# Kernel optimization log

Measured on AMD Instinct MI355X. Metric: run time of the kernel, lower is better.

The kernel has to match this reference:

```python
import jax, jax.numpy as jnp
import numpy as np

N_NODES = 100000
N_EDGES = 1600000
NUM_GRAPHS = 2000
IN_CH, HID = 5, 64
NEG_SLOPE = 0.2


def _lin_params(key, out_d, in_d, bias=True):
    k1, k2 = jax.random.split(key)
    bound = 1.0 / np.sqrt(in_d)
    W = jax.random.uniform(k1, (out_d, in_d), jnp.float32, -bound, bound)
    if bias:
        b = jax.random.uniform(k2, (out_d,), jnp.float32, -bound, bound)
        return W, b
    return (W,)


def setup_inputs() -> dict:
    key = jax.random.key(0)
    ks = jax.random.split(key, 12)
    x = jax.random.normal(ks[0], (N_NODES, IN_CH), jnp.float32)
    edge_index = jax.random.randint(ks[1], (2, N_EDGES), 0, N_NODES, jnp.int64)
    batch = (jnp.arange(N_NODES, dtype=jnp.int64) * NUM_GRAPHS) // N_NODES  # 50 nodes/graph, sorted
    # SAGEConv params: lin_l (on aggregated neighbors, with bias), lin_r (root, no bias)
    W1l, b1 = _lin_params(ks[2], HID, IN_CH)
    (W1r,) = _lin_params(ks[3], HID, IN_CH, bias=False)
    W2l, b2 = _lin_params(ks[4], 2 * HID, HID)
    (W2r,) = _lin_params(ks[5], 2 * HID, HID, bias=False)
    W3l, b3 = _lin_params(ks[6], 4 * HID, 2 * HID)
    (W3r,) = _lin_params(ks[7], 4 * HID, 2 * HID, bias=False)
    # classifier MLP: 512 -> 128 -> 64 -> 1
    Wc1, bc1 = _lin_params(ks[8], 2 * HID, 8 * HID)
    Wc2, bc2 = _lin_params(ks[9], HID, 2 * HID)
    Wc3, bc3 = _lin_params(ks[10], 1, HID)
    return {
        "x": x, "edge_index": edge_index, "batch": batch, "num_graphs": NUM_GRAPHS,
        "W1l": W1l, "b1": b1, "W1r": W1r,
        "W2l": W2l, "b2": b2, "W2r": W2r,
        "W3l": W3l, "b3": b3, "W3r": W3r,
        "Wc1": Wc1, "bc1": bc1, "Wc2": Wc2, "bc2": bc2, "Wc3": Wc3, "bc3": bc3,
    }


def _sage_conv(x, src, dst, Wl, b, Wr):
    # mean-aggregate messages x[src] at dst, then lin_l(agg) + lin_r(x)
    n = x.shape[0]
    s = jax.ops.segment_sum(x[src], dst, num_segments=n)
    cnt = jax.ops.segment_sum(jnp.ones((src.shape[0],), x.dtype), dst, num_segments=n)
    mean = s / jnp.maximum(cnt, 1.0)[:, None]
    return mean @ Wl.T + b + x @ Wr.T


def reference(x, edge_index, batch, num_graphs,
              W1l, b1, W1r, W2l, b2, W2r, W3l, b3, W3r,
              Wc1, bc1, Wc2, bc2, Wc3, bc3):
    src, dst = edge_index[0], edge_index[1]
    lrelu = lambda h: jax.nn.leaky_relu(h, NEG_SLOPE)
    h = lrelu(_sage_conv(x, src, dst, W1l, b1, W1r))
    h = lrelu(_sage_conv(h, src, dst, W2l, b2, W2r))
    h = lrelu(_sage_conv(h, src, dst, W3l, b3, W3r))
    # global mean + max pool per graph -> [G, 512]
    s = jax.ops.segment_sum(h, batch, num_segments=num_graphs)
    cnt = jax.ops.segment_sum(jnp.ones((h.shape[0],), h.dtype), batch, num_segments=num_graphs)
    mean_p = s / jnp.maximum(cnt, 1.0)[:, None]
    max_p = jax.ops.segment_max(h, batch, num_segments=num_graphs)
    g = jnp.concatenate([mean_p, max_p], axis=1)
    # classifier (dropout = identity in eval mode)
    g = lrelu(g @ Wc1.T + bc1)
    g = lrelu(g @ Wc2.T + bc2)
    logits = g @ Wc3.T + bc3
    return logits.squeeze(-1)
```

## Files before the change

kernel.cpp:

```cpp
#include <hip/hip_runtime.h>
#include <cstdint>
#include <cstddef>

#define NEG_SLOPE 0.2f

typedef __attribute__((ext_vector_type(8))) short bh8;
typedef __attribute__((ext_vector_type(16))) float f32x16;

__device__ inline void splitf(float x, short& hi, short& lo) {
    uint32_t u = __float_as_uint(x);
    uint32_t rh = (u + 0x7FFFu + ((u >> 16) & 1u)) & 0xFFFF0000u;
    hi = (short)(rh >> 16);
    float rem = x - __uint_as_float(rh);
    uint32_t u2 = __float_as_uint(rem);
    lo = (short)((u2 + 0x7FFFu + ((u2 >> 16) & 1u)) >> 16);
}

__global__ void sentinel_kernel(float* __restrict__ out, int n) {
    int i = blockIdx.x * blockDim.x + threadIdx.x;
    if (i < n) out[i] = 12345.0f;
}

#define HIST_CH 8192
__global__ void bucket_count_kernel(const int* __restrict__ dst, int* __restrict__ bcnt,
                                    int ne, int nb) {
    __shared__ int hist[256];
    const int tid = threadIdx.x;
    hist[tid] = 0;
    __syncthreads();
    int e0 = blockIdx.x * HIST_CH;
    for (int i = tid; i < HIST_CH; i += 256) {
        int e = e0 + i;
        if (e < ne) atomicAdd(&hist[dst[e] >> 9], 1);
    }
    __syncthreads();
    if (tid < nb && hist[tid] > 0) atomicAdd(&bcnt[tid], hist[tid]);
}

__global__ void scan256_kernel(const int* __restrict__ bcnt, int* __restrict__ boff, int n) {
    const int tid = threadIdx.x, lane = tid & 63, wid = tid >> 6;
    __shared__ int wt[4];
    int v = (tid < n) ? bcnt[tid] : 0;
    int incl = v;
    #pragma unroll
    for (int o = 1; o < 64; o <<= 1) {
        int t = __shfl_up(incl, o);
        if (lane >= o) incl += t;
    }
    if (lane == 63) wt[wid] = incl;
    __syncthreads();
    if (tid < 4) {
        int w = wt[tid], winc = w;
        #pragma unroll
        for (int o = 1; o < 4; o <<= 1) {
            int t = __shfl_up(winc, o);
            if (tid >= o) winc += t;
        }
        wt[tid] = winc - w;
    }
    __syncthreads();
    int excl = wt[wid] + incl - v;
    if (tid < n) boff[tid] = excl;
    if (tid == n - 1) boff[n] = excl + v;
}

#define SCAT_CH 4096
__global__ void bucket_scatter_kernel(const int* __restrict__ src, const int* __restrict__ dst,
                                      const int* __restrict__ boff, int* __restrict__ bcur,
                                      unsigned* __restrict__ pairs, int ne, int nb) {
    __shared__ int hist[256], lcur[256], gbase[256];
    const int tid = threadIdx.x;
    hist[tid] = 0; lcur[tid] = 0;
    __syncthreads();
    int e0 = blockIdx.x * SCAT_CH;
    for (int i = tid; i < SCAT_CH; i += 256) {
        int e = e0 + i;
        if (e < ne) atomicAdd(&hist[dst[e] >> 9], 1);
    }
    __syncthreads();
    if (tid < nb) {
        int h = hist[tid];
        gbase[tid] = (h > 0) ? (boff[tid] + atomicAdd(&bcur[tid], h)) : 0;
    }
    __syncthreads();
    for (int i = tid; i < SCAT_CH; i += 256) {
        int e = e0 + i;
        if (e < ne) {
            int d = dst[e];
            int b = d >> 9;
            int r = atomicAdd(&lcur[b], 1);
            pairs[gbase[b] + r] = ((unsigned)(d & 511) << 17) | (unsigned)src[e];
        }
    }
}

__global__ __launch_bounds__(512) void bucket_sort_kernel(
        const unsigned* __restrict__ pairs, const int* __restrict__ boff,
        int* __restrict__ off, int* __restrict__ csr, int n_nodes) {
    __shared__ int cnt[512], lcur[512];
    __shared__ int wt[8];
    const int b = blockIdx.x;
    const int tid = threadIdx.x, lane = tid & 63, wid = tid >> 6;
    const int s = boff[b], t = boff[b + 1];
    cnt[tid] = 0; lcur[tid] = 0;
    __syncthreads();
    for (int i = s + tid; i < t; i += 512)
        atomicAdd(&cnt[pairs[i] >> 17], 1);
    __syncthreads();
    int v = cnt[tid];
    int incl = v;
    #pragma unroll
    for (int o = 1; o < 64; o <<= 1) {
        int tt = __shfl_up(incl, o);
        if (lane >= o) incl += tt;
    }
    if (lane == 63) wt[wid] = incl;
    __syncthreads();
    if (tid < 8) {
        int w = wt[tid], winc = w;
        #pragma unroll
        for (int o = 1; o < 8; o <<= 1) {
            int tt = __shfl_up(winc, o);
            if (tid >= o) winc += tt;
        }
        wt[tid] = winc - w;
    }
    __syncthreads();
    int excl = wt[wid] + incl - v;
    __syncthreads();
    cnt[tid] = excl;
    int node = b * 512 + tid;
    if (node < n_nodes) off[node] = s + excl;
    if (b == 0 && tid == 0) off[n_nodes] = boff[gridDim.x];
    __syncthreads();
    for (int i = s + tid; i < t; i += 512) {
        unsigned p = pairs[i];
        int bin = p >> 17;
        int r = atomicAdd(&lcur[bin], 1);
        csr[s + cnt[bin] + r] = (int)(p & 0x1FFFFu);
    }
}

__global__ void pack_wsplit_kernel(const float* __restrict__ Wl, const float* __restrict__ Wr,
                                   short* __restrict__ Whi, short* __restrict__ Wlo,
                                   int COUT, int K, int CIN) {
    int i = blockIdx.x * blockDim.x + threadIdx.x;
    if (i >= COUT * K) return;
    int n = i / K, k = i % K;
    float v = (k < CIN) ? Wl[n * CIN + k] : Wr[n * CIN + (k - CIN)];
    short h, l;
    splitf(v, h, l);
    Whi[i] = h; Wlo[i] = l;
}

__global__ __launch_bounds__(256) void sage1_kernel(
        const float* __restrict__ x, const int* __restrict__ off,
        const int* __restrict__ csr, const float* __restrict__ W1l,
        const float* __restrict__ W1r, const float* __restrict__ b1,
        unsigned short* __restrict__ h1hi, unsigned short* __restrict__ h1lo,
        int n_nodes) {
    __shared__ float sWl[320], sWr[320], sb[64];
    const int tid = threadIdx.x;
    for (int i = tid; i < 320; i += 256) { sWl[i] = W1l[i]; sWr[i] = W1r[i]; }
    if (tid < 64) sb[tid] = b1[tid];
    __syncthreads();
    int node = blockIdx.x * 4 + (tid >> 6);
    int lane = tid & 63;
    if (node >= n_nodes) return;
    int slot = lane >> 3, cg = lane & 7;
    int e0 = off[node], cnt = off[node + 1] - e0;
    float a0 = 0.f, a1 = 0.f;
    int i = slot;
    for (; i + 8 < cnt; i += 16) {
        int s0 = csr[e0 + i];
        int s1 = csr[e0 + i + 8];
        a0 += (cg < 5) ? x[(size_t)s0 * 5 + cg] : 0.f;
        a1 += (cg < 5) ? x[(size_t)s1 * 5 + cg] : 0.f;
    }
    for (; i < cnt; i += 8) {
        int s = csr[e0 + i];
        a0 += (cg < 5) ? x[(size_t)s * 5 + cg] : 0.f;
    }
    float acc = a0 + a1;
    #pragma unroll
    for (int o = 8; o < 64; o <<= 1) acc += __shfl_xor(acc, o);
    float inv = (cnt > 0) ? 1.f / (float)cnt : 0.f;
    float m = acc * inv;
    float xv = (lane < 5) ? x[(size_t)node * 5 + lane] : 0.f;
    float o = sb[lane];
    #pragma unroll
    for (int c = 0; c < 5; ++c) {
        o += sWl[lane * 5 + c] * __shfl(m, c);
        o += sWr[lane * 5 + c] * __shfl(xv, c);
    }
    o = o > 0.f ? o : o * NEG_SLOPE;
    short h, l;
    splitf(o, h, l);
    h1hi[(size_t)node * 64 + lane] = (unsigned short)h;
    h1lo[(size_t)node * 64 + lane] = (unsigned short)l;
}

template<int CIN>
__global__ void agg_bf16_kernel(const unsigned short* __restrict__ hb,
                                const int* __restrict__ off, const int* __restrict__ csr,
                                unsigned short* __restrict__ mhi,
                                unsigned short* __restrict__ mlo, int n_nodes) {
    constexpr int LPR = CIN / 8;
    constexpr int SLOTS = 64 / LPR;
    constexpr int UN = 16 / SLOTS;
    int node = blockIdx.x * (blockDim.x >> 6) + (threadIdx.x >> 6);
    int lane = threadIdx.x & 63;
    if (node >= n_nodes) return;
    int slot = lane / LPR, cg = lane % LPR;
    int e0 = off[node], cnt = off[node + 1] - e0;
    const unsigned short* base = hb + cg * 8;
    float acc[UN][8];
    #pragma unroll
    for (int u = 0; u < UN; ++u)
        #pragma unroll
        for (int k = 0; k < 8; ++k) acc[u][k] = 0.f;
    int i = slot;
    for (; i + (UN - 1) * SLOTS < cnt; i += UN * SLOTS) {
        int s[UN];
        #pragma unroll
        for (int u = 0; u < UN; ++u) s[u] = csr[e0 + i + u * SLOTS];
        uint4 v[UN];
        #pragma unroll
        for (int u = 0; u < UN; ++u)
            v[u] = *(const uint4*)(base + (size_t)s[u] * CIN);
        #pragma unroll
        for (int u = 0; u < UN; ++u) {
            unsigned w0 = v[u].x, w1 = v[u].y, w2 = v[u].z, w3 = v[u].w;
            acc[u][0] += __uint_as_float(w0 << 16);
            acc[u][1] += __uint_as_float(w0 & 0xFFFF0000u);
            acc[u][2] += __uint_as_float(w1 << 16);
            acc[u][3] += __uint_as_float(w1 & 0xFFFF0000u);
            acc[u][4] += __uint_as_float(w2 << 16);
            acc[u][5] += __uint_as_float(w2 & 0xFFFF0000u);
            acc[u][6] += __uint_as_float(w3 << 16);
            acc[u][7] += __uint_as_float(w3 & 0xFFFF0000u);
        }
    }
    for (; i < cnt; i += SLOTS) {
        uint4 v = *(const uint4*)(base + (size_t)csr[e0 + i] * CIN);
        unsigned w0 = v.x, w1 = v.y, w2 = v.z, w3 = v.w;
        acc[0][0] += __uint_as_float(w0 << 16);
        acc[0][1] += __uint_as_float(w0 & 0xFFFF0000u);
        acc[0][2] += __uint_as_float(w1 << 16);
        acc[0][3] += __uint_as_float(w1 & 0xFFFF0000u);
        acc[0][4] += __uint_as_float(w2 << 16);
        acc[0][5] += __uint_as_float(w2 & 0xFFFF0000u);
        acc[0][6] += __uint_as_float(w3 << 16);
        acc[0][7] += __uint_as_float(w3 & 0xFFFF0000u);
    }
    float r[8];
    #pragma unroll
    for (int k = 0; k < 8; ++k) {
        float s = acc[0][k];
        #pragma unroll
        for (int u = 1; u < UN; ++u) s += acc[u][k];
        r[k] = s;
    }
    #pragma unroll
    for (int o = LPR; o < 64; o <<= 1)
        #pragma unroll
        for (int k = 0; k < 8; ++k) r[k] += __shfl_xor(r[k], o);
    if (slot == 0) {
        float inv = (cnt > 0) ? 1.f / (float)cnt : 0.f;
        bh8 ho, lo8;
        #pragma unroll
        for (int k = 0; k < 8; ++k) {
            short a, b;
            splitf(r[k] * inv, a, b);
            ho[k] = a; lo8[k] = b;
        }
        size_t idx = (size_t)node * CIN + cg * 8;
        *(bh8*)&mhi[idx] = ho;
        *(bh8*)&mlo[idx] = lo8;
    }
}

#define BM 128
#define BN 64
#define BK 16

template<bool RELU>
__global__ __launch_bounds__(256) void gemm_cat_kernel(
        const float* __restrict__ AL, const float* __restrict__ AR,
        const float* __restrict__ W, const float* __restrict__ bias,
        float* __restrict__ C, int M, int N, int K, int CIN) {
    __shared__ float As[BK][BM + 4];
    __shared__ float Bs[BK][BN + 4];
    const int row0 = blockIdx.x * BM;
    const int col0 = blockIdx.y * BN;
    const int tid = threadIdx.x;
    const int ttm = tid & 15, ttn = tid >> 4;

    float acc[8][4];
    #pragma unroll
    for (int i = 0; i < 8; ++i)
        #pragma unroll
        for (int j = 0; j < 4; ++j) acc[i][j] = 0.f;

    for (int k0 = 0; k0 < K; k0 += BK) {
        for (int i = tid; i < BM * BK; i += 256) {
            int m = i >> 4, k = i & 15;
            int r = row0 + m, kk = k0 + k;
            float v = 0.f;
            if (r < M && kk < K)
                v = (kk < CIN) ? AL[(size_t)r * CIN + kk]
                               : AR[(size_t)r * CIN + (kk - CIN)];
            As[k][m] = v;
        }
        for (int i = tid; i < BN * BK; i += 256) {
            int n = i >> 4, k = i & 15;
            int c = col0 + n, kk = k0 + k;
            Bs[k][n] = (c < N && kk < K) ? W[(size_t)c * K + kk] : 0.f;
        }
        __syncthreads();
        #pragma unroll
        for (int k = 0; k < BK; ++k) {
            float4 a0 = *(const float4*)&As[k][ttm * 8];
            float4 a1 = *(const float4*)&As[k][ttm * 8 + 4];
            float4 b0 = *(const float4*)&Bs[k][ttn * 4];
            float av[8] = {a0.x, a0.y, a0.z, a0.w, a1.x, a1.y, a1.z, a1.w};
            float bv[4] = {b0.x, b0.y, b0.z, b0.w};
            #pragma unroll
            for (int i = 0; i < 8; ++i)
                #pragma unroll
                for (int j = 0; j < 4; ++j)
                    acc[i][j] += av[i] * bv[j];
        }
        __syncthreads();
    }

    float bv[4];
    #pragma unroll
    for (int j = 0; j < 4; ++j) bv[j] = bias[col0 + ttn * 4 + j];
    #pragma unroll
    for (int i = 0; i < 8; ++i) {
        int r = row0 + ttm * 8 + i;
        if (r < M) {
            float t0 = acc[i][0] + bv[0];
            float t1 = acc[i][1] + bv[1];
            float t2 = acc[i][2] + bv[2];
            float t3 = acc[i][3] + bv[3];
            if (RELU) {
                t0 = t0 > 0.f ? t0 : t0 * NEG_SLOPE;
                t1 = t1 > 0.f ? t1 : t1 * NEG_SLOPE;
                t2 = t2 > 0.f ? t2 : t2 * NEG_SLOPE;
                t3 = t3 > 0.f ? t3 : t3 * NEG_SLOPE;
            }
            float4 v; v.x = t0; v.y = t1; v.z = t2; v.w = t3;
            *(float4*)&C[(size_t)r * N + col0 + ttn * 4] = v;
        }
    }
}

__global__ __launch_bounds__(256) void gemm_cat_mfma_ps_kernel(
        const unsigned short* __restrict__ ALhi, const unsigned short* __restrict__ ALlo,
        const unsigned short* __restrict__ ARhi, const unsigned short* __restrict__ ARlo,
        const short* __restrict__ Whi, const short* __restrict__ Wlo,
        const float* __restrict__ bias,
        unsigned short* __restrict__ Chi, unsigned short* __restrict__ Clo,
        int M, int N, int K, int CIN) {
    __shared__ short AsH[128][40], AsL[128][40];
    __shared__ short BsH[128][40], BsL[128][40];
    const int row0 = blockIdx.x * 128;
    const int n0 = blockIdx.y * 128;
    const int tid = threadIdx.x;
    const int w = tid >> 6;
    const int lane31 = tid & 31, lhalf = (tid & 63) >> 5;

    f32x16 acc[4];
    #pragma unroll
    for (int ci = 0; ci < 4; ++ci)
        #pragma unroll
        for (int r = 0; r < 16; ++r) acc[ci][r] = 0.f;

    for (int k0 = 0; k0 < K; k0 += 32) {
        const unsigned short* Ahi = (k0 < CIN) ? ALhi : ARhi;
        const unsigned short* Alo = (k0 < CIN) ? ALlo : ARlo;
        const int kb = (k0 < CIN) ? k0 : k0 - CIN;
        {
            int row = tid >> 1, kq = (tid & 1) * 16;
            int r = row0 + row;
            uint4 h0 = {0,0,0,0}, h1v = {0,0,0,0}, l0 = {0,0,0,0}, l1 = {0,0,0,0};
            if (r < M) {
                const uint4* ph = (const uint4*)&Ahi[(size_t)r * CIN + kb + kq];
                const uint4* pl = (const uint4*)&Alo[(size_t)r * CIN + kb + kq];
                h0 = ph[0]; h1v = ph[1];
                l0 = pl[0]; l1 = pl[1];
            }
            *(uint4*)&AsH[row][kq] = h0;  *(uint4*)&AsH[row][kq + 8] = h1v;
            *(uint4*)&AsL[row][kq] = l0;  *(uint4*)&AsL[row][kq + 8] = l1;
        }
        {
            int n = tid & 127, half = tid >> 7;
            const short* src = half ? Wlo : Whi;
            const uint4* p = (const uint4*)&src[(size_t)(n0 + n) * K + k0];
            if (half) {
                #pragma unroll
                for (int q = 0; q < 4; ++q) *(uint4*)&BsL[n][q * 8] = p[q];
            } else {
                #pragma unroll
                for (int q = 0; q < 4; ++q) *(uint4*)&BsH[n][q * 8] = p[q];
            }
        }
        __syncthreads();
        #pragma unroll
        for (int ks = 0; ks < 2; ++ks) {
            int kofs = ks * 16 + lhalf * 8;
            bh8 aH = *(bh8*)&AsH[w * 32 + lane31][kofs];
            bh8 aL = *(bh8*)&AsL[w * 32 + lane31][kofs];
            #pragma unroll
            for (int ci = 0; ci < 4; ++ci) {
                bh8 bH = *(bh8*)&BsH[ci * 32 + lane31][kofs];
                bh8 bL = *(bh8*)&BsL[ci * 32 + lane31][kofs];
                acc[ci] = __builtin_amdgcn_mfma_f32_32x32x16_bf16(aH, bH, acc[ci], 0, 0, 0);
                acc[ci] = __builtin_amdgcn_mfma_f32_32x32x16_bf16(aH, bL, acc[ci], 0, 0, 0);
                acc[ci] = __builtin_amdgcn_mfma_f32_32x32x16_bf16(aL, bH, acc[ci], 0, 0, 0);
            }
        }
        __syncthreads();
    }

    #pragma unroll
    for (int ci = 0; ci < 4; ++ci) {
        int col = n0 + ci * 32 + lane31;
        float b = bias[col];
        #pragma unroll
        for (int r = 0; r < 16; ++r) {
            int row = row0 + w * 32 + (r & 3) + 8 * (r >> 2) + 4 * lhalf;
            if (row < M) {
                float v = acc[ci][r] + b;
                v = v > 0.f ? v : v * NEG_SLOPE;
                short h, l;
                splitf(v, h, l);
                Chi[(size_t)row * N + col] = (unsigned short)h;
                Clo[(size_t)row * N + col] = (unsigned short)l;
            }
        }
    }
}

__global__ __launch_bounds__(256) void gemm_cat_mfma_kernel(
        const float* __restrict__ AL, const float* __restrict__ AR,
        const short* __restrict__ Whi, const short* __restrict__ Wlo,
        const float* __restrict__ bias, float* __restrict__ C,
        int M, int N, int K, int CIN) {
    __shared__ short AsH[128][40], AsL[128][40];
    __shared__ short BsH[128][40], BsL[128][40];
    const int row0 = blockIdx.x * 128;
    const int n0 = blockIdx.y * 128;
    const int tid = threadIdx.x;
    const int w = tid >> 6;
    const int lane31 = tid & 31, lhalf = (tid & 63) >> 5;

    f32x16 acc[4];
    #pragma unroll
    for (int ci = 0; ci < 4; ++ci)
        #pragma unroll
        for (int r = 0; r < 16; ++r) acc[ci][r] = 0.f;

    for (int k0 = 0; k0 < K; k0 += 32) {
        const float* Asrc = (k0 < CIN) ? AL : AR;
        const int kb = (k0 < CIN) ? k0 : k0 - CIN;
        {
            int row = tid >> 1, kq = (tid & 1) * 16;
            int r = row0 + row;
            float vv[16];
            #pragma unroll
            for (int i = 0; i < 16; ++i) vv[i] = 0.f;
            if (r < M) {
                const float* p = &Asrc[(size_t)r * CIN + kb + kq];
                #pragma unroll
                for (int q = 0; q < 4; ++q) {
                    float4 v = ((const float4*)p)[q];
                    vv[q * 4 + 0] = v.x; vv[q * 4 + 1] = v.y;
                    vv[q * 4 + 2] = v.z; vv[q * 4 + 3] = v.w;
                }
            }
            #pragma unroll
            for (int half = 0; half < 2; ++half) {
                bh8 h8, l8;
                #pragma unroll
                for (int i = 0; i < 8; ++i) {
                    short a, b;
                    splitf(vv[half * 8 + i], a, b);
                    h8[i] = a; l8[i] = b;
                }
                *(bh8*)&AsH[row][kq + half * 8] = h8;
                *(bh8*)&AsL[row][kq + half * 8] = l8;
            }
        }
        {
            int n = tid & 127, half = tid >> 7;
            const short* src = half ? Wlo : Whi;
            const uint4* p = (const uint4*)&src[(size_t)(n0 + n) * K + k0];
            if (half) {
                #pragma unroll
                for (int q = 0; q < 4; ++q) *(uint4*)&BsL[n][q * 8] = p[q];
            } else {
                #pragma unroll
                for (int q = 0; q < 4; ++q) *(uint4*)&BsH[n][q * 8] = p[q];
            }
        }
        __syncthreads();
        #pragma unroll
        for (int ks = 0; ks < 2; ++ks) {
            int kofs = ks * 16 + lhalf * 8;
            bh8 aH = *(bh8*)&AsH[w * 32 + lane31][kofs];
            bh8 aL = *(bh8*)&AsL[w * 32 + lane31][kofs];
            #pragma unroll
            for (int ci = 0; ci < 4; ++ci) {
                bh8 bH = *(bh8*)&BsH[ci * 32 + lane31][kofs];
                bh8 bL = *(bh8*)&BsL[ci * 32 + lane31][kofs];
                acc[ci] = __builtin_amdgcn_mfma_f32_32x32x16_bf16(aH, bH, acc[ci], 0, 0, 0);
                acc[ci] = __builtin_amdgcn_mfma_f32_32x32x16_bf16(aH, bL, acc[ci], 0, 0, 0);
                acc[ci] = __builtin_amdgcn_mfma_f32_32x32x16_bf16(aL, bH, acc[ci], 0, 0, 0);
            }
        }
        __syncthreads();
    }

    #pragma unroll
    for (int ci = 0; ci < 4; ++ci) {
        int col = n0 + ci * 32 + lane31;
        float b = bias[col];
        #pragma unroll
        for (int r = 0; r < 16; ++r) {
            int row = row0 + w * 32 + (r & 3) + 8 * (r >> 2) + 4 * lhalf;
            if (row < M) {
                float v = acc[ci][r] + b;
                v = v > 0.f ? v : v * NEG_SLOPE;
                C[(size_t)row * N + col] = v;
            }
        }
    }
}

template<int CIN>
__global__ __launch_bounds__(512) void gemm_pool_mfma4_kernel(
        const unsigned short* __restrict__ ALhi, const unsigned short* __restrict__ ALlo,
        const unsigned short* __restrict__ ARhi, const unsigned short* __restrict__ ARlo,
        const short* __restrict__ Whi, const short* __restrict__ Wlo,
        const float* __restrict__ bias, float* __restrict__ gout,
        int npg, int NCH) {
    __shared__ short AsH[128][24], AsL[128][24];
    __shared__ short BsH[256][24], BsL[256][24];
    const int g2 = blockIdx.x * 2;
    constexpr int K = 2 * CIN;
    constexpr int NT = K / 16;
    const int tid = threadIdx.x;
    const int w = tid >> 6;
    const int lane31 = tid & 31, lhalf = (tid & 63) >> 5;
    const int gi = w & 1;
    const int rt0 = gi * 2;
    const int cb = (w >> 1) * 2;
    const int arow = tid >> 2, akq = (tid & 3) * 4;
    const int agrow = arow >> 6, ar = arow & 63;
    const int bn = tid & 255, bhalf = tid >> 8;

    f32x16 acc[2][2];
    #pragma unroll
    for (int ri = 0; ri < 2; ++ri)
        #pragma unroll
        for (int ci = 0; ci < 2; ++ci)
            #pragma unroll
            for (int r = 0; r < 16; ++r) acc[ri][ci][r] = 0.f;

    const size_t abase = ((size_t)(g2 + agrow) * npg + ar) * CIN + akq;
    const short* srcw = bhalf ? Wlo : Whi;

    uint2 cAh = {0,0}, cAl = {0,0};
    uint4 cB0, cB1;
    {
        if (ar < npg) {
            cAh = *(const uint2*)&ALhi[abase];
            cAl = *(const uint2*)&ALlo[abase];
        }
        const uint4* pb = (const uint4*)&srcw[(size_t)bn * K];
        cB0 = pb[0]; cB1 = pb[1];
    }

    #pragma unroll
    for (int t = 0; t < NT; ++t) {
        *(uint2*)&AsH[arow][akq] = cAh;
        *(uint2*)&AsL[arow][akq] = cAl;
        if (bhalf) {
            *(uint4*)&BsL[bn][0] = cB0; *(uint4*)&BsL[bn][8] = cB1;
        } else {
            *(uint4*)&BsH[bn][0] = cB0; *(uint4*)&BsH[bn][8] = cB1;
        }
        __syncthreads();
        uint2 nAh = {0,0}, nAl = {0,0};
        uint4 nB0 = {0,0,0,0}, nB1 = {0,0,0,0};
        if (t + 1 < NT) {
            const int k0 = (t + 1) * 16;
            const unsigned short* Ahi = (k0 < CIN) ? ALhi : ARhi;
            const unsigned short* Alo = (k0 < CIN) ? ALlo : ARlo;
            const int kb = (k0 < CIN) ? k0 : k0 - CIN;
            if (ar < npg) {
                nAh = *(const uint2*)&Ahi[abase + kb];
                nAl = *(const uint2*)&Alo[abase + kb];
            }
            const uint4* pb = (const uint4*)&srcw[(size_t)bn * K + k0];
            nB0 = pb[0]; nB1 = pb[1];
        }
        {
            int kofs = lhalf * 8;
            bh8 aH0 = *(bh8*)&AsH[(rt0 + 0) * 32 + lane31][kofs];
            bh8 aL0 = *(bh8*)&AsL[(rt0 + 0) * 32 + lane31][kofs];
            bh8 aH1 = *(bh8*)&AsH[(rt0 + 1) * 32 + lane31][kofs];
            bh8 aL1 = *(bh8*)&AsL[(rt0 + 1) * 32 + lane31][kofs];
            #pragma unroll
            for (int ci = 0; ci < 2; ++ci) {
                bh8 bH = *(bh8*)&BsH[(cb + ci) * 32 + lane31][kofs];
                bh8 bL = *(bh8*)&BsL[(cb + ci) * 32 + lane31][kofs];
                acc[0][ci] = __builtin_amdgcn_mfma_f32_32x32x16_bf16(aH0, bH, acc[0][ci], 0, 0, 0);
                acc[0][ci] = __builtin_amdgcn_mfma_f32_32x32x16_bf16(aH0, bL, acc[0][ci], 0, 0, 0);
                acc[0][ci] = __builtin_amdgcn_mfma_f32_32x32x16_bf16(aL0, bH, acc[0][ci], 0, 0, 0);
                acc[1][ci] = __builtin_amdgcn_mfma_f32_32x32x16_bf16(aH1, bH, acc[1][ci], 0, 0, 0);
                acc[1][ci] = __builtin_amdgcn_mfma_f32_32x32x16_bf16(aH1, bL, acc[1][ci], 0, 0, 0);
                acc[1][ci] = __builtin_amdgcn_mfma_f32_32x32x16_bf16(aL1, bH, acc[1][ci], 0, 0, 0);
            }
        }
        __syncthreads();
        if (t + 1 < NT) { cAh = nAh; cAl = nAl; cB0 = nB0; cB1 = nB1; }
    }

    float (*redS)[258] = (float(*)[258])&AsH[0][0];
    float (*redM)[258] = (float(*)[258])&AsL[0][0];

    #pragma unroll
    for (int ci = 0; ci < 2; ++ci) {
        int col = (cb + ci) * 32 + lane31;
        float b = bias[col];
        float ls = 0.f, lm = -__builtin_huge_valf();
        #pragma unroll
        for (int ri = 0; ri < 2; ++ri) {
            #pragma unroll
            for (int r = 0; r < 16; ++r) {
                int crow = (r & 3) + 8 * (r >> 2) + 4 * lhalf;
                int grow = ri * 32 + crow;
                if (grow < npg) {
                    float v = acc[ri][ci][r] + b;
                    v = v > 0.f ? v : v * NEG_SLOPE;
                    ls += v;
                    lm = fmaxf(lm, v);
                }
            }
        }
        ls += __shfl_xor(ls, 32);
        lm = fmaxf(lm, __shfl_xor(lm, 32));
        if (lhalf == 0) { redS[gi][col] = ls; redM[gi][col] = lm; }
    }
    __syncthreads();
    {
        int c = tid & 255, gi2 = tid >> 8;
        float s = redS[gi2][c];
        float m = redM[gi2][c];
        gout[(size_t)(g2 + gi2) * (2 * NCH) + c] = s / (float)npg;
        gout[(size_t)(g2 + gi2) * (2 * NCH) + NCH + c] = m;
    }
}

__global__ void final_kernel(const float* __restrict__ c2, const float* __restrict__ Wc3,
                             const float* __restrict__ bc3, float* __restrict__ out, int G) {
    int g = blockIdx.x * (blockDim.x >> 6) + (threadIdx.x >> 6);
    int lane = threadIdx.x & 63;
    if (g >= G) return;
    float v = c2[(size_t)g * 64 + lane] * Wc3[lane];
    #pragma unroll
    for (int o = 32; o > 0; o >>= 1) v += __shfl_down(v, o);
    if (lane == 0) out[g] = v + bc3[0];
}

extern "C" void kernel_launch(void* const* d_in, const int* in_sizes, int n_in,
                              void* d_out, int out_size, void* d_ws, size_t ws_size,
                              hipStream_t stream) {
    const float* x   = (const float*)d_in[0];
    const int* ei    = (const int*)d_in[1];
    const float* W1l = (const float*)d_in[4];
    const float* b1  = (const float*)d_in[5];
    const float* W1r = (const float*)d_in[6];
    const float* W2l = (const float*)d_in[7];
    const float* b2  = (const float*)d_in[8];
    const float* W2r = (const float*)d_in[9];
    const float* W3l = (const float*)d_in[10];
    const float* b3  = (const float*)d_in[11];
    const float* W3r = (const float*)d_in[12];
    const float* Wc1 = (const float*)d_in[13];
    const float* bc1 = (const float*)d_in[14];
    const float* Wc2 = (const float*)d_in[15];
    const float* bc2 = (const float*)d_in[16];
    const float* Wc3 = (const float*)d_in[17];
    const float* bc3 = (const float*)d_in[18];
    float* out = (float*)d_out;

    const int nodes = in_sizes[0] / 5;
    const int ne    = in_sizes[1] / 2;
    const int G     = out_size;
    const int npg   = nodes / G;
    const int nb    = (nodes + 511) >> 9;

    char* ws = (char*)d_ws;
    size_t pos = 0;
    auto take = [&](size_t bytes) -> char* {
        char* p = ws + pos;
        pos += (bytes + 255) & ~(size_t)255;
        return p;
    };
    int* off     = (int*)take((size_t)(nodes + 1) * 4);
    int* csr     = (int*)take((size_t)ne * 4);
    int* bcnt    = (int*)take(256 * 4);
    int* bcur    = (int*)take(256 * 4);
    int* boff    = (int*)take(257 * 4);
    short* Whi2  = (short*)take((size_t)128 * 128 * 2);
    short* Wlo2  = (short*)take((size_t)128 * 128 * 2);
    short* Whi3  = (short*)take((size_t)256 * 256 * 2);
    short* Wlo3  = (short*)take((size_t)256 * 256 * 2);
    short* WhiC  = (short*)take((size_t)128 * 512 * 2);
    short* WloC  = (short*)take((size_t)128 * 512 * 2);
    float* gbuf  = (float*)take((size_t)G * 512 * 4);
    float* c1    = (float*)take((size_t)G * 128 * 4);
    float* c2    = (float*)take((size_t)G * 64 * 4);
    unsigned short* m1hi = (unsigned short*)take((size_t)nodes * 64 * 2);
    unsigned short* m1lo = (unsigned short*)take((size_t)nodes * 64 * 2);
    unsigned short* h1hi = (unsigned short*)take((size_t)nodes * 64 * 2);
    unsigned short* h1lo = (unsigned short*)take((size_t)nodes * 64 * 2);
    unsigned short* h2hi = (unsigned short*)take((size_t)nodes * 128 * 2);
    unsigned short* h2lo = (unsigned short*)take((size_t)nodes * 128 * 2);
    unsigned short* m2hi = m1hi;
    unsigned short* m2lo = h1hi;
    unsigned* pairs = (unsigned*)m1hi;

    if (pos > ws_size) {
        sentinel_kernel<<<(G + 255) / 256, 256, 0, stream>>>(out, G);
        return;
    }

    const int* src = ei;
    const int* dst = ei + ne;

    hipMemsetAsync(bcnt, 0, 512 * 4, stream);

    bucket_count_kernel<<<(ne + HIST_CH - 1) / HIST_CH, 256, 0, stream>>>(dst, bcnt, ne, nb);
    scan256_kernel<<<1, 256, 0, stream>>>(bcnt, boff, nb);
    bucket_scatter_kernel<<<(ne + SCAT_CH - 1) / SCAT_CH, 256, 0, stream>>>(
        src, dst, boff, bcur, pairs, ne, nb);
    bucket_sort_kernel<<<nb, 512, 0, stream>>>(pairs, boff, off, csr, nodes);

    pack_wsplit_kernel<<<(128 * 128 + 255) / 256, 256, 0, stream>>>(W2l, W2r, Whi2, Wlo2, 128, 128, 64);
    pack_wsplit_kernel<<<(256 * 256 + 255) / 256, 256, 0, stream>>>(W3l, W3r, Whi3, Wlo3, 256, 256, 128);
    pack_wsplit_kernel<<<(128 * 512 + 255) / 256, 256, 0, stream>>>(Wc1, Wc1, WhiC, WloC, 128, 512, 512);

    sage1_kernel<<<(nodes + 3) / 4, 256, 0, stream>>>(x, off, csr, W1l, W1r, b1,
                                                      h1hi, h1lo, nodes);

    agg_bf16_kernel<64><<<(nodes + 3) / 4, 256, 0, stream>>>(h1hi, off, csr, m1hi, m1lo, nodes);
    {
        dim3 g((nodes + 127) / 128, 1);
        gemm_cat_mfma_ps_kernel<<<g, 256, 0, stream>>>(m1hi, m1lo, h1hi, h1lo,
                                                       Whi2, Wlo2, b2, h2hi, h2lo,
                                                       nodes, 128, 128, 64);
    }
    agg_bf16_kernel<128><<<(nodes + 3) / 4, 256, 0, stream>>>(h2hi, off, csr, m2hi, m2lo, nodes);
    gemm_pool_mfma4_kernel<128><<<G / 2, 512, 0, stream>>>(m2hi, m2lo, h2hi, h2lo,
                                                           Whi3, Wlo3, b3, gbuf, npg, 256);
    {
        dim3 g((G + 127) / 128, 1);
        gemm_cat_mfma_kernel<<<g, 256, 0, stream>>>(gbuf, gbuf, WhiC, WloC, bc1, c1,
                                                    G, 128, 512, 512);
    }
    {
        dim3 g((G + BM - 1) / BM, 64 / BN);
        gemm_cat_kernel<true><<<g, 256, 0, stream>>>(c1, nullptr, Wc2, bc2, c2, G, 64, 128, 128);
    }
    final_kernel<<<(G + 3) / 4, 256, 0, stream>>>(c2, Wc3, bc3, out, G);
}
```

Baseline: 396.1 us.

## Process one graph per 256-thread block in fused layer-3 GEMM+pool kernel

Changes the fused third-layer GEMM and pooling kernel from two graphs per 512-thread block to one graph per 256-thread block, giving twice as many smaller blocks. Each thread now loads both the hi and lo halves of the weight tile. This should improve occupancy and load balance across CUs and shrink shared memory per block. The cost is that each weight tile is reloaded from L2 twice as often, since it is no longer shared between two graphs.

```diff
diff --git a/kernel.cpp b/kernel.cpp
--- a/kernel.cpp
+++ b/kernel.cpp
@@ -541,26 +541,23 @@
 }
 
 template<int CIN>
-__global__ __launch_bounds__(512) void gemm_pool_mfma4_kernel(
+__global__ __launch_bounds__(256) void gemm_pool_mfma5_kernel(
         const unsigned short* __restrict__ ALhi, const unsigned short* __restrict__ ALlo,
         const unsigned short* __restrict__ ARhi, const unsigned short* __restrict__ ARlo,
         const short* __restrict__ Whi, const short* __restrict__ Wlo,
         const float* __restrict__ bias, float* __restrict__ gout,
         int npg, int NCH) {
-    __shared__ short AsH[128][24], AsL[128][24];
+    __shared__ short AsH[64][24], AsL[64][24];
     __shared__ short BsH[256][24], BsL[256][24];
-    const int g2 = blockIdx.x * 2;
+    const int g = blockIdx.x;
     constexpr int K = 2 * CIN;
     constexpr int NT = K / 16;
     const int tid = threadIdx.x;
     const int w = tid >> 6;
     const int lane31 = tid & 31, lhalf = (tid & 63) >> 5;
-    const int gi = w & 1;
-    const int rt0 = gi * 2;
-    const int cb = (w >> 1) * 2;
+    const int cb = w * 2;
     const int arow = tid >> 2, akq = (tid & 3) * 4;
-    const int agrow = arow >> 6, ar = arow & 63;
-    const int bn = tid & 255, bhalf = tid >> 8;
+    const int bn = tid;
 
     f32x16 acc[2][2];
     #pragma unroll
@@ -570,50 +567,50 @@
             #pragma unroll
             for (int r = 0; r < 16; ++r) acc[ri][ci][r] = 0.f;
 
-    const size_t abase = ((size_t)(g2 + agrow) * npg + ar) * CIN + akq;
-    const short* srcw = bhalf ? Wlo : Whi;
+    const size_t abase = ((size_t)g * npg + arow) * CIN + akq;
 
     uint2 cAh = {0,0}, cAl = {0,0};
-    uint4 cB0, cB1;
+    uint4 cBh0, cBh1, cBl0, cBl1;
     {
-        if (ar < npg) {
+        if (arow < npg) {
             cAh = *(const uint2*)&ALhi[abase];
             cAl = *(const uint2*)&ALlo[abase];
         }
-        const uint4* pb = (const uint4*)&srcw[(size_t)bn * K];
-        cB0 = pb[0]; cB1 = pb[1];
+        const uint4* ph = (const uint4*)&Whi[(size_t)bn * K];
+        const uint4* pl = (const uint4*)&Wlo[(size_t)bn * K];
+        cBh0 = ph[0]; cBh1 = ph[1];
+        cBl0 = pl[0]; cBl1 = pl[1];
     }
 
     #pragma unroll
     for (int t = 0; t < NT; ++t) {
         *(uint2*)&AsH[arow][akq] = cAh;
         *(uint2*)&AsL[arow][akq] = cAl;
-        if (bhalf) {
-            *(uint4*)&BsL[bn][0] = cB0; *(uint4*)&BsL[bn][8] = cB1;
-        } else {
-            *(uint4*)&BsH[bn][0] = cB0; *(uint4*)&BsH[bn][8] = cB1;
-        }
+        *(uint4*)&BsH[bn][0] = cBh0; *(uint4*)&BsH[bn][8] = cBh1;
+        *(uint4*)&BsL[bn][0] = cBl0; *(uint4*)&BsL[bn][8] = cBl1;
         __syncthreads();
         uint2 nAh = {0,0}, nAl = {0,0};
-        uint4 nB0 = {0,0,0,0}, nB1 = {0,0,0,0};
+        uint4 nBh0 = {0,0,0,0}, nBh1 = {0,0,0,0}, nBl0 = {0,0,0,0}, nBl1 = {0,0,0,0};
         if (t + 1 < NT) {
             const int k0 = (t + 1) * 16;
             const unsigned short* Ahi = (k0 < CIN) ? ALhi : ARhi;
             const unsigned short* Alo = (k0 < CIN) ? ALlo : ARlo;
             const int kb = (k0 < CIN) ? k0 : k0 - CIN;
-            if (ar < npg) {
+            if (arow < npg) {
                 nAh = *(const uint2*)&Ahi[abase + kb];
                 nAl = *(const uint2*)&Alo[abase + kb];
             }
-            const uint4* pb = (const uint4*)&srcw[(size_t)bn * K + k0];
-            nB0 = pb[0]; nB1 = pb[1];
+            const uint4* ph = (const uint4*)&Whi[(size_t)bn * K + k0];
+            const uint4* pl = (const uint4*)&Wlo[(size_t)bn * K + k0];
+            nBh0 = ph[0]; nBh1 = ph[1];
+            nBl0 = pl[0]; nBl1 = pl[1];
         }
         {
             int kofs = lhalf * 8;
-            bh8 aH0 = *(bh8*)&AsH[(rt0 + 0) * 32 + lane31][kofs];
-            bh8 aL0 = *(bh8*)&AsL[(rt0 + 0) * 32 + lane31][kofs];
-            bh8 aH1 = *(bh8*)&AsH[(rt0 + 1) * 32 + lane31][kofs];
-            bh8 aL1 = *(bh8*)&AsL[(rt0 + 1) * 32 + lane31][kofs];
+            bh8 aH0 = *(bh8*)&AsH[lane31][kofs];
+            bh8 aL0 = *(bh8*)&AsL[lane31][kofs];
+            bh8 aH1 = *(bh8*)&AsH[32 + lane31][kofs];
+            bh8 aL1 = *(bh8*)&AsL[32 + lane31][kofs];
             #pragma unroll
             for (int ci = 0; ci < 2; ++ci) {
                 bh8 bH = *(bh8*)&BsH[(cb + ci) * 32 + lane31][kofs];
@@ -627,11 +624,14 @@
             }
         }
         __syncthreads();
-        if (t + 1 < NT) { cAh = nAh; cAl = nAl; cB0 = nB0; cB1 = nB1; }
-    }
-
-    float (*redS)[258] = (float(*)[258])&AsH[0][0];
-    float (*redM)[258] = (float(*)[258])&AsL[0][0];
+        if (t + 1 < NT) {
+            cAh = nAh; cAl = nAl;
+            cBh0 = nBh0; cBh1 = nBh1; cBl0 = nBl0; cBl1 = nBl1;
+        }
+    }
+
+    float* redS = (float*)&AsH[0][0];
+    float* redM = (float*)&AsL[0][0];
 
     #pragma unroll
     for (int ci = 0; ci < 2; ++ci) {
@@ -654,15 +654,13 @@
         }
         ls += __shfl_xor(ls, 32);
         lm = fmaxf(lm, __shfl_xor(lm, 32));
-        if (lhalf == 0) { redS[gi][col] = ls; redM[gi][col] = lm; }
+        if (lhalf == 0) { redS[col] = ls; redM[col] = lm; }
     }
     __syncthreads();
     {
-        int c = tid & 255, gi2 = tid >> 8;
-        float s = redS[gi2][c];
-        float m = redM[gi2][c];
-        gout[(size_t)(g2 + gi2) * (2 * NCH) + c] = s / (float)npg;
-        gout[(size_t)(g2 + gi2) * (2 * NCH) + NCH + c] = m;
+        int c = tid;
+        gout[(size_t)g * (2 * NCH) + c] = redS[c] / (float)npg;
+        gout[(size_t)g * (2 * NCH) + NCH + c] = redM[c];
     }
 }
 
@@ -767,8 +765,8 @@
                                                        nodes, 128, 128, 64);
     }
     agg_bf16_kernel<128><<<(nodes + 3) / 4, 256, 0, stream>>>(h2hi, off, csr, m2hi, m2lo, nodes);
-    gemm_pool_mfma4_kernel<128><<<G / 2, 512, 0, stream>>>(m2hi, m2lo, h2hi, h2lo,
-                                                           Whi3, Wlo3, b3, gbuf, npg, 256);
+    gemm_pool_mfma5_kernel<128><<<G, 256, 0, stream>>>(m2hi, m2lo, h2hi, h2lo,
+                                                       Whi3, Wlo3, b3, gbuf, npg, 256);
     {
         dim3 g((G + 127) / 128, 1);
         gemm_cat_mfma_kernel<<<g, 256, 0, stream>>>(gbuf, gbuf, WhiC, WloC, bc1, c1,
```

After: 419.0 us. 1.06x slower.
